# Kernel optimization log

Hardware: AMD Instinct MI355X
Metric: run time of the kernel (lower is better)

The kernel has to match this reference:

```python
import jax, jax.numpy as jnp
import numpy as np

B, S, HID = 2, 2048, 2048
H, HKV, DH = 32, 8, 64
GROUPS = H // HKV
SCALE = DH ** -0.5
ROPE_THETA = 10000.0
NEG_INF = jnp.finfo(jnp.float32).min


def setup_inputs() -> dict:
    key = jax.random.key(0)
    ks = jax.random.split(key, 6)
    hidden_states = jax.random.normal(ks[0], (B, S, HID), dtype=jnp.float32)
    # true rotary embeddings (HF Llama style): inv_freq over half dim, duplicated
    inv_freq = 1.0 / (ROPE_THETA ** (np.arange(0, DH, 2, dtype=np.float32) / DH))
    freqs = np.arange(S, dtype=np.float32)[:, None] * inv_freq[None, :]  # [S, DH/2]
    emb = np.concatenate([freqs, freqs], axis=-1)                        # [S, DH]
    cos = jnp.broadcast_to(jnp.asarray(np.cos(emb), jnp.float32), (B, S, DH))
    sin = jnp.broadcast_to(jnp.asarray(np.sin(emb), jnp.float32), (B, S, DH))
    # additive causal mask [1,1,S,S]
    causal = jnp.tril(jnp.ones((S, S), dtype=bool))
    attention_mask = jnp.where(causal, 0.0, NEG_INF)[None, None].astype(jnp.float32)
    std = 0.02
    Wq = jax.random.normal(ks[1], (H * DH, HID), dtype=jnp.float32) * std
    Wk = jax.random.normal(ks[2], (HKV * DH, HID), dtype=jnp.float32) * std
    Wv = jax.random.normal(ks[3], (HKV * DH, HID), dtype=jnp.float32) * std
    Wo = jax.random.normal(ks[4], (HID, H * DH), dtype=jnp.float32) * std
    return {"hidden_states": hidden_states, "cos": cos, "sin": sin,
            "attention_mask": attention_mask, "Wq": Wq, "Wk": Wk, "Wv": Wv, "Wo": Wo}


def _rotate_half(x):
    x1, x2 = jnp.split(x, 2, axis=-1)
    return jnp.concatenate([-x2, x1], axis=-1)


def reference(hidden_states, cos, sin, attention_mask, Wq, Wk, Wv, Wo):
    b, s, _ = hidden_states.shape
    # projections -> [B, H(kv), S, DH]
    q = (hidden_states @ Wq.T).reshape(b, s, H, DH).transpose(0, 2, 1, 3)
    k = (hidden_states @ Wk.T).reshape(b, s, HKV, DH).transpose(0, 2, 1, 3)
    v = (hidden_states @ Wv.T).reshape(b, s, HKV, DH).transpose(0, 2, 1, 3)
    # RoPE (cos/sin: [B,S,DH] -> broadcast over head axis)
    c = cos[:, None, :, :]
    sn = sin[:, None, :, :]
    q = q * c + _rotate_half(q) * sn
    k = k * c + _rotate_half(k) * sn
    # GQA: repeat kv heads
    k = jnp.repeat(k, GROUPS, axis=1)  # [B,H,S,DH]
    v = jnp.repeat(v, GROUPS, axis=1)
    # eager attention: full [B,H,S,S] scores in memory
    scores = jnp.einsum('bhqd,bhkd->bhqk', q, k) * SCALE + attention_mask[:, :, :, :s]
    attn = jax.nn.softmax(scores, axis=-1)
    out = jnp.einsum('bhqk,bhkd->bhqd', attn, v)
    out = out.transpose(0, 2, 1, 3).reshape(b, s, H * DH)
    return out @ Wo.T
```

## Files before the change

kernel.cpp:

```cpp
#include <hip/hip_runtime.h>
#include <hip/hip_bf16.h>
#include <cstdint>
#include <cstddef>

#define B_    2
#define S_    2048
#define HID_  2048
#define H_    32
#define HKV_  8
#define DH_   64
#define SC2_  0.1803368801111244f

typedef __bf16 bf16;
typedef bf16  bf16x2 __attribute__((ext_vector_type(2)));
typedef bf16  bf16x4 __attribute__((ext_vector_type(4)));
typedef bf16  bf16x8 __attribute__((ext_vector_type(8)));
typedef float f32x4  __attribute__((ext_vector_type(4)));
typedef float f32x16 __attribute__((ext_vector_type(16)));
typedef uint32_t u32x2 __attribute__((ext_vector_type(2)));

typedef __attribute__((address_space(3))) uint32_t  lds_u32_t;
typedef __attribute__((address_space(1))) const uint32_t glob_u32_t;

__device__ __forceinline__ void async16(const void* g, void* l) {
    __builtin_amdgcn_global_load_lds((glob_u32_t*)g, (lds_u32_t*)l, 16, 0, 0);
}

__device__ __forceinline__ bf16x8 cvt8(float4 a, float4 b) {
    bf16x8 r;
    r[0] = (bf16)a.x; r[1] = (bf16)a.y; r[2] = (bf16)a.z; r[3] = (bf16)a.w;
    r[4] = (bf16)b.x; r[5] = (bf16)b.y; r[6] = (bf16)b.z; r[7] = (bf16)b.w;
    return r;
}

__device__ __forceinline__ uint32_t pkbf(float a, float b) {
    bf16x2 t; t[0] = (bf16)a; t[1] = (bf16)b;
    return __builtin_bit_cast(uint32_t, t);
}
__device__ __forceinline__ bf16x8 mk8(uint32_t a, uint32_t b, uint32_t c, uint32_t d) {
    union { uint32_t u[4]; bf16x8 v; } t;
    t.u[0] = a; t.u[1] = b; t.u[2] = c; t.u[3] = d;
    return t.v;
}

__global__ __launch_bounds__(256) void cvt_all_kernel(
    const float* __restrict__ X,  const float* __restrict__ Wq,
    const float* __restrict__ Wk, const float* __restrict__ Wv,
    const float* __restrict__ Wo,
    bf16* __restrict__ Xb,  bf16* __restrict__ Wqb, bf16* __restrict__ Wkb,
    bf16* __restrict__ Wvb, bf16* __restrict__ Wob)
{
    const int i = blockIdx.x * 256 + threadIdx.x;
    const float* src; bf16* dst; int off;
    if (i < 1048576)      { src = X;  dst = Xb;  off = i; }
    else if (i < 1572864) { src = Wq; dst = Wqb; off = i - 1048576; }
    else if (i < 1703936) { src = Wk; dst = Wkb; off = i - 1572864; }
    else if (i < 1835008) { src = Wv; dst = Wvb; off = i - 1703936; }
    else                  { src = Wo; dst = Wob; off = i - 1835008; }
    float4 a = ((const float4*)src)[2 * off];
    float4 b = ((const float4*)src)[2 * off + 1];
    ((bf16x8*)dst)[off] = cvt8(a, b);
}

__global__ __launch_bounds__(256) void gemm_qkv_kernel(
    const bf16* __restrict__ A,
    const bf16* __restrict__ Wqb, const bf16* __restrict__ Wkb,
    const bf16* __restrict__ Wvb,
    const float* __restrict__ cs, const float* __restrict__ sn,
    bf16* __restrict__ Qo, bf16* __restrict__ Ko, bf16* __restrict__ Vt)
{
    __shared__ bf16 a_lds[2][128 * 64];
    __shared__ bf16 b_lds[2][128 * 64];

    const int tid  = threadIdx.x;
    const int wave = tid >> 6;
    const int lane = tid & 63;
    const int quad = lane >> 4;
    const int l16  = lane & 15;
    const int wm   = wave >> 1;
    const int wn   = wave & 1;

    const int idx = blockIdx.x + 32 * blockIdx.y;
    const int swz = (idx & 7) * 96 + (idx >> 3);
    const int m0  = (swz & 31) * 128;
    const int n0  = (swz >> 5) * 128;

    f32x4 acc[4][4];
    #pragma unroll
    for (int mt = 0; mt < 4; ++mt)
        #pragma unroll
        for (int nt = 0; nt < 4; ++nt)
            acc[mt][nt] = (f32x4){0.f, 0.f, 0.f, 0.f};

    int srow[4], sgcol[4];
    const bf16* browp[4];
    #pragma unroll
    for (int i = 0; i < 4; ++i) {
        const int e = tid * 8 + i * 2048;
        srow[i] = e >> 6;
        const int chunk = (e >> 3) & 7;
        sgcol[i] = (chunk ^ (srow[i] & 7)) << 3;
        const int n = n0 + srow[i];
        browp[i] = (n < 2048) ? (Wqb + (size_t)n * HID_)
                 : (n < 2560) ? (Wkb + (size_t)(n - 2048) * HID_)
                              : (Wvb + (size_t)(n - 2560) * HID_);
    }

    #pragma unroll
    for (int i = 0; i < 4; ++i) {
        async16(A + (size_t)(m0 + srow[i]) * HID_ + sgcol[i],
                &a_lds[0][tid * 8 + i * 2048]);
        async16(browp[i] + sgcol[i],
                &b_lds[0][tid * 8 + i * 2048]);
    }
    __syncthreads();

    for (int k0 = 0; k0 < HID_; k0 += 64) {
        const int cur = (k0 >> 6) & 1;
        if (k0 + 64 < HID_) {
            #pragma unroll
            for (int i = 0; i < 4; ++i) {
                async16(A + (size_t)(m0 + srow[i]) * HID_ + k0 + 64 + sgcol[i],
                        &a_lds[cur ^ 1][tid * 8 + i * 2048]);
                async16(browp[i] + k0 + 64 + sgcol[i],
                        &b_lds[cur ^ 1][tid * 8 + i * 2048]);
            }
        }
        const bf16* al = a_lds[cur];
        const bf16* bl = b_lds[cur];
        #pragma unroll
        for (int ks = 0; ks < 2; ++ks) {
            bf16x8 af[4], bfr[4];
            #pragma unroll
            for (int mt = 0; mt < 4; ++mt) {
                const int row = wm * 64 + mt * 16 + l16;
                const int c = (ks * 4 + quad) ^ (row & 7);
                af[mt] = *(const bf16x8*)(&al[row * 64 + c * 8]);
            }
            #pragma unroll
            for (int nt = 0; nt < 4; ++nt) {
                const int row = wn * 64 + nt * 16 + l16;
                const int c = (ks * 4 + quad) ^ (row & 7);
                bfr[nt] = *(const bf16x8*)(&bl[row * 64 + c * 8]);
            }
            #pragma unroll
            for (int mt = 0; mt < 4; ++mt)
                #pragma unroll
                for (int nt = 0; nt < 4; ++nt)
                    acc[mt][nt] = __builtin_amdgcn_mfma_f32_16x16x32_bf16(
                        af[mt], bfr[nt], acc[mt][nt], 0, 0, 0);
        }
        __syncthreads();
    }

    const int nw = n0 + wn * 64;
    const int d  = l16;
    #pragma unroll
    for (int mt = 0; mt < 4; ++mt) {
        #pragma unroll
        for (int r = 0; r < 4; ++r) {
            const int m  = m0 + wm * 64 + mt * 16 + quad * 4 + r;
            const int bb = m >> 11;
            const int ss = m & (S_ - 1);
            const float v0 = acc[mt][0][r], v1 = acc[mt][1][r];
            const float v2 = acc[mt][2][r], v3 = acc[mt][3][r];
            if (nw < 2048) {
                const int h = nw >> 6;
                bf16* dp = Qo + ((size_t)(bb * H_ + h) * S_ + ss) * DH_;
                const float* cp = cs + ((size_t)bb * S_ + ss) * DH_;
                const float* sp = sn + ((size_t)bb * S_ + ss) * DH_;
                dp[ 0 + d] = (bf16)((v0 * cp[ 0 + d] - v2 * sp[ 0 + d]) * SC2_);
                dp[16 + d] = (bf16)((v1 * cp[16 + d] - v3 * sp[16 + d]) * SC2_);
                dp[32 + d] = (bf16)((v2 * cp[32 + d] + v0 * sp[32 + d]) * SC2_);
                dp[48 + d] = (bf16)((v3 * cp[48 + d] + v1 * sp[48 + d]) * SC2_);
            } else if (nw < 2560) {
                const int h = (nw - 2048) >> 6;
                bf16* dp = Ko + ((size_t)(bb * HKV_ + h) * S_ + ss) * DH_;
                const float* cp = cs + ((size_t)bb * S_ + ss) * DH_;
                const float* sp = sn + ((size_t)bb * S_ + ss) * DH_;
                dp[ 0 + d] = (bf16)(v0 * cp[ 0 + d] - v2 * sp[ 0 + d]);
                dp[16 + d] = (bf16)(v1 * cp[16 + d] - v3 * sp[16 + d]);
                dp[32 + d] = (bf16)(v2 * cp[32 + d] + v0 * sp[32 + d]);
                dp[48 + d] = (bf16)(v3 * cp[48 + d] + v1 * sp[48 + d]);
            } else {
                const int h = (nw - 2560) >> 6;
                bf16* dp = Vt + ((size_t)(bb * HKV_ + h) * DH_) * S_ + ss;
                dp[(size_t)( 0 + d) * S_] = (bf16)v0;
                dp[(size_t)(16 + d) * S_] = (bf16)v1;
                dp[(size_t)(32 + d) * S_] = (bf16)v2;
                dp[(size_t)(48 + d) * S_] = (bf16)v3;
            }
        }
    }
}

__global__ __launch_bounds__(256) void gemm_out_kernel(
    const bf16* __restrict__ A, const bf16* __restrict__ Wb,
    float* __restrict__ Y)
{
    __shared__ bf16 a_lds[2][128 * 64];
    __shared__ bf16 b_lds[2][128 * 64];

    const int tid  = threadIdx.x;
    const int wave = tid >> 6;
    const int lane = tid & 63;
    const int quad = lane >> 4;
    const int l16  = lane & 15;
    const int wm   = wave >> 1;
    const int wn   = wave & 1;

    const int idx = blockIdx.x + 32 * blockIdx.y;
    const int swz = (idx & 7) * 64 + (idx >> 3);
    const int m0  = (swz & 31) * 128;
    const int n0  = (swz >> 5) * 128;

    f32x4 acc[4][4];
    #pragma unroll
    for (int mt = 0; mt < 4; ++mt)
        #pragma unroll
        for (int nt = 0; nt < 4; ++nt)
            acc[mt][nt] = (f32x4){0.f, 0.f, 0.f, 0.f};

    int srow[4], sgcol[4];
    #pragma unroll
    for (int i = 0; i < 4; ++i) {
        const int e = tid * 8 + i * 2048;
        srow[i] = e >> 6;
        const int chunk = (e >> 3) & 7;
        sgcol[i] = (chunk ^ (srow[i] & 7)) << 3;
    }

    #pragma unroll
    for (int i = 0; i < 4; ++i) {
        async16(A + (size_t)(m0 + srow[i]) * HID_ + sgcol[i],
                &a_lds[0][tid * 8 + i * 2048]);
        async16(Wb + (size_t)(n0 + srow[i]) * HID_ + sgcol[i],
                &b_lds[0][tid * 8 + i * 2048]);
    }
    __syncthreads();

    for (int k0 = 0; k0 < HID_; k0 += 64) {
        const int cur = (k0 >> 6) & 1;
        if (k0 + 64 < HID_) {
            #pragma unroll
            for (int i = 0; i < 4; ++i) {
                async16(A + (size_t)(m0 + srow[i]) * HID_ + k0 + 64 + sgcol[i],
                        &a_lds[cur ^ 1][tid * 8 + i * 2048]);
                async16(Wb + (size_t)(n0 + srow[i]) * HID_ + k0 + 64 + sgcol[i],
                        &b_lds[cur ^ 1][tid * 8 + i * 2048]);
            }
        }
        const bf16* al = a_lds[cur];
        const bf16* bl = b_lds[cur];
        #pragma unroll
        for (int ks = 0; ks < 2; ++ks) {
            bf16x8 af[4], bfr[4];
            #pragma unroll
            for (int mt = 0; mt < 4; ++mt) {
                const int row = wm * 64 + mt * 16 + l16;
                const int c = (ks * 4 + quad) ^ (row & 7);
                af[mt] = *(const bf16x8*)(&al[row * 64 + c * 8]);
            }
            #pragma unroll
            for (int nt = 0; nt < 4; ++nt) {
                const int row = wn * 64 + nt * 16 + l16;
                const int c = (ks * 4 + quad) ^ (row & 7);
                bfr[nt] = *(const bf16x8*)(&bl[row * 64 + c * 8]);
            }
            #pragma unroll
            for (int mt = 0; mt < 4; ++mt)
                #pragma unroll
                for (int nt = 0; nt < 4; ++nt)
                    acc[mt][nt] = __builtin_amdgcn_mfma_f32_16x16x32_bf16(
                        af[mt], bfr[nt], acc[mt][nt], 0, 0, 0);
        }
        __syncthreads();
    }

    #pragma unroll
    for (int mt = 0; mt < 4; ++mt)
        #pragma unroll
        for (int nt = 0; nt < 4; ++nt)
            #pragma unroll
            for (int r = 0; r < 4; ++r) {
                const int m = m0 + wm * 64 + mt * 16 + quad * 4 + r;
                const int n = n0 + wn * 64 + nt * 16 + l16;
                Y[(size_t)m * HID_ + n] = acc[mt][nt][r];
            }
}

__global__ __launch_bounds__(256) void attn_kernel(
    const bf16* __restrict__ Q, const bf16* __restrict__ K,
    const bf16* __restrict__ Vt, bf16* __restrict__ O)
{
    __shared__ bf16 k_lds[2][64 * 64];
    __shared__ bf16 v_lds[2][64 * 64];

    const int tid  = threadIdx.x;
    const int wave = tid >> 6;
    const int lane = tid & 63;
    const int l32  = lane & 31;
    const int half = lane >> 5;

    const int j  = blockIdx.x;
    const int g  = j >> 8;
    const int p  = j & 255;
    const int s  = p >> 6;
    const int bh = p & 63;
    const int h  = bh & 31;
    const int b  = bh >> 5;
    int qt;
    if      (g == 0) qt = 15 - s;
    else if (g == 1) qt = 8 + s;
    else if (g == 2) qt = 7 - s;
    else             qt = s;
    const int hkv = h >> 2;

    const bf16* Qg = Q  + (size_t)(b * H_ + h) * S_ * DH_;
    const bf16* Kg = K  + (size_t)(b * HKV_ + hkv) * S_ * DH_;
    const bf16* Vg = Vt + ((size_t)(b * HKV_ + hkv) * DH_) * S_;

    const int srow0  = tid >> 3;
    const int scolsw = ((tid & 7) ^ ((tid >> 3) & 7)) << 3;

    const int qb0 = qt * 128 + wave * 32;
    const int qa  = qb0 + l32;
    const int nkt = 2 * qt + 2;

    bf16x8 qf[4];
    #pragma unroll
    for (int c = 0; c < 4; ++c)
        qf[c] = *(const bf16x8*)(Qg + (size_t)qa * DH_ + c * 16 + half * 8);

    f32x16 o_acc[2];
    #pragma unroll
    for (int dt = 0; dt < 2; ++dt)
        #pragma unroll
        for (int e = 0; e < 16; ++e) o_acc[dt][e] = 0.f;
    float m_i = -1e30f, l_i = 0.f;

    #pragma unroll
    for (int i = 0; i < 2; ++i) {
        const int row = srow0 + i * 32;
        async16(Kg + (size_t)row * DH_ + scolsw, &k_lds[0][tid * 8 + i * 2048]);
        async16(Vg + (size_t)row * S_  + scolsw, &v_lds[0][tid * 8 + i * 2048]);
    }
    __syncthreads();

    for (int kt = 0; kt < nkt; ++kt) {
        if (kt + 1 < nkt) {
            bf16* kb = k_lds[(kt + 1) & 1];
            bf16* vb = v_lds[(kt + 1) & 1];
            #pragma unroll
            for (int i = 0; i < 2; ++i) {
                const int row = srow0 + i * 32;
                async16(Kg + (size_t)((kt + 1) * 64 + row) * DH_ + scolsw,
                        kb + tid * 8 + i * 2048);
                async16(Vg + (size_t)row * S_ + (kt + 1) * 64 + scolsw,
                        vb + tid * 8 + i * 2048);
            }
        }

        if (kt * 64 <= qb0 + 31) {
            const bf16* kb = k_lds[kt & 1];
            const bf16* vb = v_lds[kt & 1];
            const bool act1 = (kt * 64 + 32) <= (qb0 + 31);

            f32x16 s0, s1;
            {
                bf16x8 kf[4];
                #pragma unroll
                for (int c = 0; c < 4; ++c) {
                    const int col = ((2 * c + half) ^ (l32 & 7)) << 3;
                    kf[c] = *(const bf16x8*)(kb + l32 * 64 + col);
                }
                f32x16 a;
                #pragma unroll
                for (int e = 0; e < 16; ++e) a[e] = 0.f;
                __builtin_amdgcn_s_setprio(1);
                #pragma unroll
                for (int c = 0; c < 4; ++c)
                    a = __builtin_amdgcn_mfma_f32_32x32x16_bf16(kf[c], qf[c], a, 0, 0, 0);
                __builtin_amdgcn_s_setprio(0);
                s0 = a;
            }
            if (act1) {
                bf16x8 kf[4];
                #pragma unroll
                for (int c = 0; c < 4; ++c) {
                    const int row = 32 + l32;
                    const int col = ((2 * c + half) ^ (row & 7)) << 3;
                    kf[c] = *(const bf16x8*)(kb + row * 64 + col);
                }
                f32x16 a;
                #pragma unroll
                for (int e = 0; e < 16; ++e) a[e] = 0.f;
                __builtin_amdgcn_s_setprio(1);
                #pragma unroll
                for (int c = 0; c < 4; ++c)
                    a = __builtin_amdgcn_mfma_f32_32x32x16_bf16(kf[c], qf[c], a, 0, 0, 0);
                __builtin_amdgcn_s_setprio(0);
                s1 = a;
            }

            if (!((kt * 64 + 31) <= qb0)) {
                const int qrel = qa - kt * 64 - 4 * half;
                #pragma unroll
                for (int e = 0; e < 16; ++e)
                    if (((e & 3) + 8 * (e >> 2)) > qrel) s0[e] = -1e30f;
            }
            if (act1 && !((kt * 64 + 63) <= qb0)) {
                const int qrel = qa - kt * 64 - 32 - 4 * half;
                #pragma unroll
                for (int e = 0; e < 16; ++e)
                    if (((e & 3) + 8 * (e >> 2)) > qrel) s1[e] = -1e30f;
            }

            float mx = s0[0];
            #pragma unroll
            for (int e = 1; e < 16; ++e) mx = fmaxf(mx, s0[e]);
            if (act1)
                #pragma unroll
                for (int e = 0; e < 16; ++e) mx = fmaxf(mx, s1[e]);
            mx = fmaxf(mx, __shfl_xor(mx, 32));

            float al = 1.f;
            if (!__all(mx <= m_i + 8.f)) {
                const float mn = fmaxf(m_i, mx);
                al = exp2f(m_i - mn);
                m_i = mn;
                #pragma unroll
                for (int dt = 0; dt < 2; ++dt)
                    #pragma unroll
                    for (int e = 0; e < 16; ++e) o_acc[dt][e] *= al;
            }

            float sm = 0.f;
            #pragma unroll
            for (int e = 0; e < 16; ++e) {
                const float pp = exp2f(s0[e] - m_i);
                s0[e] = pp; sm += pp;
            }
            if (act1)
                #pragma unroll
                for (int e = 0; e < 16; ++e) {
                    const float pp = exp2f(s1[e] - m_i);
                    s1[e] = pp; sm += pp;
                }
            sm += __shfl_xor(sm, 32);
            l_i = l_i * al + sm;

            bf16x8 pf[4];
            {
                uint32_t d0 = pkbf(s0[0],  s0[1]),  d1 = pkbf(s0[2],  s0[3]);
                uint32_t d2 = pkbf(s0[4],  s0[5]),  d3 = pkbf(s0[6],  s0[7]);
                uint32_t d4 = pkbf(s0[8],  s0[9]),  d5 = pkbf(s0[10], s0[11]);
                uint32_t d6 = pkbf(s0[12], s0[13]), d7 = pkbf(s0[14], s0[15]);
                u32x2 r02 = __builtin_amdgcn_permlane32_swap(d0, d2, false, false);
                u32x2 r13 = __builtin_amdgcn_permlane32_swap(d1, d3, false, false);
                u32x2 r46 = __builtin_amdgcn_permlane32_swap(d4, d6, false, false);
                u32x2 r57 = __builtin_amdgcn_permlane32_swap(d5, d7, false, false);
                pf[0] = mk8(r02[0], r13[0], r02[1], r13[1]);
                pf[1] = mk8(r46[0], r57[0], r46[1], r57[1]);
            }
            if (act1) {
                uint32_t d0 = pkbf(s1[0],  s1[1]),  d1 = pkbf(s1[2],  s1[3]);
                uint32_t d2 = pkbf(s1[4],  s1[5]),  d3 = pkbf(s1[6],  s1[7]);
                uint32_t d4 = pkbf(s1[8],  s1[9]),  d5 = pkbf(s1[10], s1[11]);
                uint32_t d6 = pkbf(s1[12], s1[13]), d7 = pkbf(s1[14], s1[15]);
                u32x2 r02 = __builtin_amdgcn_permlane32_swap(d0, d2, false, false);
                u32x2 r13 = __builtin_amdgcn_permlane32_swap(d1, d3, false, false);
                u32x2 r46 = __builtin_amdgcn_permlane32_swap(d4, d6, false, false);
                u32x2 r57 = __builtin_amdgcn_permlane32_swap(d5, d7, false, false);
                pf[2] = mk8(r02[0], r13[0], r02[1], r13[1]);
                pf[3] = mk8(r46[0], r57[0], r46[1], r57[1]);
            }

            bf16x8 vf[2][4];
            #pragma unroll
            for (int dt = 0; dt < 2; ++dt)
                #pragma unroll
                for (int c = 0; c < 4; ++c) {
                    const int row = dt * 32 + l32;
                    const int col = ((2 * c + half) ^ (row & 7)) << 3;
                    vf[dt][c] = *(const bf16x8*)(vb + row * 64 + col);
                }

            const int nc = act1 ? 4 : 2;
            __builtin_amdgcn_s_setprio(1);
            #pragma unroll
            for (int c = 0; c < 4; ++c) {
                if (c >= nc) break;
                #pragma unroll
                for (int dt = 0; dt < 2; ++dt)
                    o_acc[dt] = __builtin_amdgcn_mfma_f32_32x32x16_bf16(
                        vf[dt][c], pf[c], o_acc[dt], 0, 0, 0);
            }
            __builtin_amdgcn_s_setprio(0);
        }
        __syncthreads();
    }

    const float inv = 1.f / l_i;
    bf16* op = O + ((size_t)(b * S_ + qa) * H_ + h) * DH_;
    #pragma unroll
    for (int dt = 0; dt < 2; ++dt)
        #pragma unroll
        for (int g2 = 0; g2 < 4; ++g2) {
            bf16x4 ov;
            #pragma unroll
            for (int r = 0; r < 4; ++r) ov[r] = (bf16)(o_acc[dt][g2 * 4 + r] * inv);
            *(bf16x4*)(op + dt * 32 + g2 * 8 + half * 4) = ov;
        }
}

extern "C" void kernel_launch(void* const* d_in, const int* in_sizes, int n_in,
                              void* d_out, int out_size, void* d_ws, size_t ws_size,
                              hipStream_t stream)
{
    const float* X    = (const float*)d_in[0];
    const float* cs   = (const float*)d_in[1];
    const float* sn   = (const float*)d_in[2];
    const float* Wq   = (const float*)d_in[4];
    const float* Wk   = (const float*)d_in[5];
    const float* Wv   = (const float*)d_in[6];
    const float* Wo   = (const float*)d_in[7];
    float* Y          = (float*)d_out;

    bf16* Xb  = (bf16*)d_ws;
    bf16* Wqb = Xb  + (size_t)8388608;
    bf16* Wkb = Wqb + (size_t)4194304;
    bf16* Wvb = Wkb + (size_t)1048576;
    bf16* Wob = Wvb + (size_t)1048576;
    bf16* Qb  = Wob + (size_t)4194304;
    bf16* Kb  = Qb  + (size_t)8388608;
    bf16* Vtb = Kb  + (size_t)2097152;
    bf16* Ob  = Vtb + (size_t)2097152;

    dim3 blk(256);
    cvt_all_kernel<<<dim3(9216), blk, 0, stream>>>(X, Wq, Wk, Wv, Wo,
                                                   Xb, Wqb, Wkb, Wvb, Wob);
    gemm_qkv_kernel<<<dim3(32, 24), blk, 0, stream>>>(Xb, Wqb, Wkb, Wvb,
                                                      cs, sn, Qb, Kb, Vtb);
    attn_kernel<<<dim3(1024), blk, 0, stream>>>(Qb, Kb, Vtb, Ob);
    gemm_out_kernel<<<dim3(32, 16), blk, 0, stream>>>(Ob, Wob, Y);
}
```

Baseline: 350.3 us.

## Give each attention wave its own private K/V pipeline with paired query strips

Each wave now owns a private double-buffered K/V LDS region and streams 32-key tiles independently with vmcnt waits, removing the block-wide __syncthreads and the skipped tiles where some waves idled past their causal limit. Each wave handles two 32-row query strips (qs and 63-qs) in turn to balance causal work, and the grid is halved to 512 blocks. In exchange, K/V loads are no longer shared across the four waves, so global/L2 traffic per block roughly quadruples, and LDS use grows to 64KB, which may limit occupancy.

```diff
diff --git a/kernel.cpp b/kernel.cpp
--- a/kernel.cpp
+++ b/kernel.cpp
@@ -293,8 +293,7 @@
     const bf16* __restrict__ Q, const bf16* __restrict__ K,
     const bf16* __restrict__ Vt, bf16* __restrict__ O)
 {
-    __shared__ bf16 k_lds[2][64 * 64];
-    __shared__ bf16 v_lds[2][64 * 64];
+    __shared__ bf16 slds[4][2][2][2048];
 
     const int tid  = threadIdx.x;
     const int wave = tid >> 6;
@@ -303,76 +302,81 @@
     const int half = lane >> 5;
 
     const int j  = blockIdx.x;
-    const int g  = j >> 8;
-    const int p  = j & 255;
-    const int s  = p >> 6;
-    const int bh = p & 63;
+    const int bh = j & 63;
     const int h  = bh & 31;
     const int b  = bh >> 5;
-    int qt;
-    if      (g == 0) qt = 15 - s;
-    else if (g == 1) qt = 8 + s;
-    else if (g == 2) qt = 7 - s;
-    else             qt = s;
+    const int kq = j >> 6;
+    const int qs1 = kq * 4 + wave;
+    const int qs2 = 63 - qs1;
     const int hkv = h >> 2;
 
     const bf16* Qg = Q  + (size_t)(b * H_ + h) * S_ * DH_;
     const bf16* Kg = K  + (size_t)(b * HKV_ + hkv) * S_ * DH_;
     const bf16* Vg = Vt + ((size_t)(b * HKV_ + hkv) * DH_) * S_;
 
-    const int srow0  = tid >> 3;
-    const int scolsw = ((tid & 7) ^ ((tid >> 3) & 7)) << 3;
-
-    const int qb0 = qt * 128 + wave * 32;
-    const int qa  = qb0 + l32;
-    const int nkt = 2 * qt + 2;
-
-    bf16x8 qf[4];
-    #pragma unroll
-    for (int c = 0; c < 4; ++c)
-        qf[c] = *(const bf16x8*)(Qg + (size_t)qa * DH_ + c * 16 + half * 8);
-
-    f32x16 o_acc[2];
-    #pragma unroll
-    for (int dt = 0; dt < 2; ++dt)
-        #pragma unroll
-        for (int e = 0; e < 16; ++e) o_acc[dt][e] = 0.f;
-    float m_i = -1e30f, l_i = 0.f;
-
-    #pragma unroll
-    for (int i = 0; i < 2; ++i) {
-        const int row = srow0 + i * 32;
-        async16(Kg + (size_t)row * DH_ + scolsw, &k_lds[0][tid * 8 + i * 2048]);
-        async16(Vg + (size_t)row * S_  + scolsw, &v_lds[0][tid * 8 + i * 2048]);
-    }
-    __syncthreads();
-
-    for (int kt = 0; kt < nkt; ++kt) {
-        if (kt + 1 < nkt) {
-            bf16* kb = k_lds[(kt + 1) & 1];
-            bf16* vb = v_lds[(kt + 1) & 1];
-            #pragma unroll
-            for (int i = 0; i < 2; ++i) {
-                const int row = srow0 + i * 32;
-                async16(Kg + (size_t)((kt + 1) * 64 + row) * DH_ + scolsw,
-                        kb + tid * 8 + i * 2048);
-                async16(Vg + (size_t)row * S_ + (kt + 1) * 64 + scolsw,
-                        vb + tid * 8 + i * 2048);
-            }
-        }
-
-        if (kt * 64 <= qb0 + 31) {
-            const bf16* kb = k_lds[kt & 1];
-            const bf16* vb = v_lds[kt & 1];
-            const bool act1 = (kt * 64 + 32) <= (qb0 + 31);
-
-            f32x16 s0, s1;
+    int krow[4], kcol[4], vdrow[4], vscol[4];
+    #pragma unroll
+    for (int i = 0; i < 4; ++i) {
+        const int t  = i * 64 + lane;
+        krow[i] = t >> 3;
+        kcol[i] = ((t & 7) ^ (krow[i] & 7)) << 3;
+        const int vj = (t & 7) ^ (krow[i] & 7);
+        vdrow[i] = krow[i] + 32 * (vj >> 2);
+        vscol[i] = (vj & 3) * 8;
+    }
+
+    #pragma unroll 1
+    for (int sp = 0; sp < 2; ++sp) {
+        const int qs  = sp ? qs2 : qs1;
+        const int qa  = qs * 32 + l32;
+        const int nkt = qs + 1;
+
+        bf16x8 qf[4];
+        #pragma unroll
+        for (int c = 0; c < 4; ++c)
+            qf[c] = *(const bf16x8*)(Qg + (size_t)qa * DH_ + c * 16 + half * 8);
+
+        f32x16 o_acc[2];
+        #pragma unroll
+        for (int dt = 0; dt < 2; ++dt)
+            #pragma unroll
+            for (int e = 0; e < 16; ++e) o_acc[dt][e] = 0.f;
+        float m_i = -1e30f, l_i = 0.f;
+
+        #pragma unroll
+        for (int i = 0; i < 4; ++i) {
+            async16(Kg + (size_t)krow[i] * DH_ + kcol[i],
+                    &slds[wave][0][0][(i * 64 + lane) * 8]);
+            async16(Vg + (size_t)vdrow[i] * S_ + vscol[i],
+                    &slds[wave][0][1][(i * 64 + lane) * 8]);
+        }
+
+        for (int kt = 0; kt < nkt; ++kt) {
+            const int cb = kt & 1;
+            if (kt + 1 < nkt) {
+                #pragma unroll
+                for (int i = 0; i < 4; ++i) {
+                    async16(Kg + (size_t)((kt + 1) * 32 + krow[i]) * DH_ + kcol[i],
+                            &slds[wave][cb ^ 1][0][(i * 64 + lane) * 8]);
+                    async16(Vg + (size_t)vdrow[i] * S_ + (kt + 1) * 32 + vscol[i],
+                            &slds[wave][cb ^ 1][1][(i * 64 + lane) * 8]);
+                }
+                asm volatile("s_waitcnt vmcnt(8)" ::: "memory");
+            } else {
+                asm volatile("s_waitcnt vmcnt(0)" ::: "memory");
+            }
+            __builtin_amdgcn_sched_barrier(0);
+
+            const bf16* kb = &slds[wave][cb][0][0];
+            const bf16* vb = &slds[wave][cb][1][0];
+
+            f32x16 s0;
             {
                 bf16x8 kf[4];
                 #pragma unroll
                 for (int c = 0; c < 4; ++c) {
-                    const int col = ((2 * c + half) ^ (l32 & 7)) << 3;
-                    kf[c] = *(const bf16x8*)(kb + l32 * 64 + col);
+                    const int ch = (2 * c + half) ^ (l32 & 7);
+                    kf[c] = *(const bf16x8*)(kb + l32 * 64 + ch * 8);
                 }
                 f32x16 a;
                 #pragma unroll
@@ -384,44 +388,17 @@
                 __builtin_amdgcn_s_setprio(0);
                 s0 = a;
             }
-            if (act1) {
-                bf16x8 kf[4];
-                #pragma unroll
-                for (int c = 0; c < 4; ++c) {
-                    const int row = 32 + l32;
-                    const int col = ((2 * c + half) ^ (row & 7)) << 3;
-                    kf[c] = *(const bf16x8*)(kb + row * 64 + col);
-                }
-                f32x16 a;
-                #pragma unroll
-                for (int e = 0; e < 16; ++e) a[e] = 0.f;
-                __builtin_amdgcn_s_setprio(1);
-                #pragma unroll
-                for (int c = 0; c < 4; ++c)
-                    a = __builtin_amdgcn_mfma_f32_32x32x16_bf16(kf[c], qf[c], a, 0, 0, 0);
-                __builtin_amdgcn_s_setprio(0);
-                s1 = a;
-            }
-
-            if (!((kt * 64 + 31) <= qb0)) {
-                const int qrel = qa - kt * 64 - 4 * half;
+
+            if (kt == qs) {
+                const int qrel = l32 - 4 * half;
                 #pragma unroll
                 for (int e = 0; e < 16; ++e)
                     if (((e & 3) + 8 * (e >> 2)) > qrel) s0[e] = -1e30f;
             }
-            if (act1 && !((kt * 64 + 63) <= qb0)) {
-                const int qrel = qa - kt * 64 - 32 - 4 * half;
-                #pragma unroll
-                for (int e = 0; e < 16; ++e)
-                    if (((e & 3) + 8 * (e >> 2)) > qrel) s1[e] = -1e30f;
-            }
 
             float mx = s0[0];
             #pragma unroll
             for (int e = 1; e < 16; ++e) mx = fmaxf(mx, s0[e]);
-            if (act1)
-                #pragma unroll
-                for (int e = 0; e < 16; ++e) mx = fmaxf(mx, s1[e]);
             mx = fmaxf(mx, __shfl_xor(mx, 32));
 
             float al = 1.f;
@@ -441,16 +418,10 @@
                 const float pp = exp2f(s0[e] - m_i);
                 s0[e] = pp; sm += pp;
             }
-            if (act1)
-                #pragma unroll
-                for (int e = 0; e < 16; ++e) {
-                    const float pp = exp2f(s1[e] - m_i);
-                    s1[e] = pp; sm += pp;
-                }
             sm += __shfl_xor(sm, 32);
             l_i = l_i * al + sm;
 
-            bf16x8 pf[4];
+            bf16x8 pf[2];
             {
                 uint32_t d0 = pkbf(s0[0],  s0[1]),  d1 = pkbf(s0[2],  s0[3]);
                 uint32_t d2 = pkbf(s0[4],  s0[5]),  d3 = pkbf(s0[6],  s0[7]);
@@ -463,55 +434,38 @@
                 pf[0] = mk8(r02[0], r13[0], r02[1], r13[1]);
                 pf[1] = mk8(r46[0], r57[0], r46[1], r57[1]);
             }
-            if (act1) {
-                uint32_t d0 = pkbf(s1[0],  s1[1]),  d1 = pkbf(s1[2],  s1[3]);
-                uint32_t d2 = pkbf(s1[4],  s1[5]),  d3 = pkbf(s1[6],  s1[7]);
-                uint32_t d4 = pkbf(s1[8],  s1[9]),  d5 = pkbf(s1[10], s1[11]);
-                uint32_t d6 = pkbf(s1[12], s1[13]), d7 = pkbf(s1[14], s1[15]);
-                u32x2 r02 = __builtin_amdgcn_permlane32_swap(d0, d2, false, false);
-                u32x2 r13 = __builtin_amdgcn_permlane32_swap(d1, d3, false, false);
-                u32x2 r46 = __builtin_amdgcn_permlane32_swap(d4, d6, false, false);
-                u32x2 r57 = __builtin_amdgcn_permlane32_swap(d5, d7, false, false);
-                pf[2] = mk8(r02[0], r13[0], r02[1], r13[1]);
-                pf[3] = mk8(r46[0], r57[0], r46[1], r57[1]);
-            }
-
-            bf16x8 vf[2][4];
+
+            bf16x8 vf[2][2];
             #pragma unroll
             for (int dt = 0; dt < 2; ++dt)
                 #pragma unroll
-                for (int c = 0; c < 4; ++c) {
-                    const int row = dt * 32 + l32;
-                    const int col = ((2 * c + half) ^ (row & 7)) << 3;
-                    vf[dt][c] = *(const bf16x8*)(vb + row * 64 + col);
+                for (int c = 0; c < 2; ++c) {
+                    const int ch = (dt * 4 + 2 * c + half) ^ (l32 & 7);
+                    vf[dt][c] = *(const bf16x8*)(vb + l32 * 64 + ch * 8);
                 }
 
-            const int nc = act1 ? 4 : 2;
             __builtin_amdgcn_s_setprio(1);
             #pragma unroll
-            for (int c = 0; c < 4; ++c) {
-                if (c >= nc) break;
+            for (int c = 0; c < 2; ++c)
                 #pragma unroll
                 for (int dt = 0; dt < 2; ++dt)
                     o_acc[dt] = __builtin_amdgcn_mfma_f32_32x32x16_bf16(
                         vf[dt][c], pf[c], o_acc[dt], 0, 0, 0);
-            }
             __builtin_amdgcn_s_setprio(0);
         }
-        __syncthreads();
-    }
-
-    const float inv = 1.f / l_i;
-    bf16* op = O + ((size_t)(b * S_ + qa) * H_ + h) * DH_;
-    #pragma unroll
-    for (int dt = 0; dt < 2; ++dt)
-        #pragma unroll
-        for (int g2 = 0; g2 < 4; ++g2) {
-            bf16x4 ov;
-            #pragma unroll
-            for (int r = 0; r < 4; ++r) ov[r] = (bf16)(o_acc[dt][g2 * 4 + r] * inv);
-            *(bf16x4*)(op + dt * 32 + g2 * 8 + half * 4) = ov;
-        }
+
+        const float inv = 1.f / l_i;
+        bf16* op = O + ((size_t)(b * S_ + qa) * H_ + h) * DH_;
+        #pragma unroll
+        for (int dt = 0; dt < 2; ++dt)
+            #pragma unroll
+            for (int g2 = 0; g2 < 4; ++g2) {
+                bf16x4 ov;
+                #pragma unroll
+                for (int r = 0; r < 4; ++r) ov[r] = (bf16)(o_acc[dt][g2 * 4 + r] * inv);
+                *(bf16x4*)(op + dt * 32 + g2 * 8 + half * 4) = ov;
+            }
+    }
 }
 
 extern "C" void kernel_launch(void* const* d_in, const int* in_sizes, int n_in,
@@ -542,6 +496,6 @@
                                                    Xb, Wqb, Wkb, Wvb, Wob);
     gemm_qkv_kernel<<<dim3(32, 24), blk, 0, stream>>>(Xb, Wqb, Wkb, Wvb,
                                                       cs, sn, Qb, Kb, Vtb);
-    attn_kernel<<<dim3(1024), blk, 0, stream>>>(Qb, Kb, Vtb, Ob);
+    attn_kernel<<<dim3(512), blk, 0, stream>>>(Qb, Kb, Vtb, Ob);
     gemm_out_kernel<<<dim3(32, 16), blk, 0, stream>>>(Ob, Wob, Y);
 }
```

Measured after the change: 355.4 us. About the same (+1.5%).
